# Performance work log

Measured on AMD Instinct MI355X. Metric: run time of the kernel, lower is better.

Reference implementation:

```python
import jax, jax.numpy as jnp
import numpy as np

NUM_HEADS = 8

def _ln(x):
    m = x.mean(-1, keepdims=True)
    v = ((x - m) ** 2).mean(-1, keepdims=True)
    return (x - m) / jnp.sqrt(v + 1e-5)

def _encoder_layer(x, qkv_w, out_w, w1, w2, attn_mask=None):
    # standard post-LN transformer encoder layer; returns output and
    # head-averaged attention probabilities (b, t, t)
    b, t, d = x.shape
    dh = d // NUM_HEADS
    qkv = jnp.einsum('btd,cde->cbte', x, qkv_w)          # (3, b, t, d)
    q, k, v = [a.reshape(b, t, NUM_HEADS, dh).transpose(0, 2, 1, 3) for a in qkv]
    scores = jnp.einsum('bhqd,bhkd->bhqk', q, k) / jnp.sqrt(jnp.asarray(dh, x.dtype))
    if attn_mask is not None:
        scores = scores + attn_mask                       # additive -inf/0 mask
    probs = jax.nn.softmax(scores, axis=-1)
    ctx = jnp.einsum('bhqk,bhkd->bhqd', probs, v)
    ctx = ctx.transpose(0, 2, 1, 3).reshape(b, t, d)
    x = _ln(x + ctx @ out_w)
    x = _ln(x + jax.nn.relu(x @ w1) @ w2)
    return x, probs.mean(axis=1)

def _window_ids(wbool):
    # faithful vectorization of generate_local_window_mask_v2's sequential scan:
    # run-length segmentation of the thresholded weights, where a run of
    # length 1 is absorbed into the following run (weights[frame_start] is
    # overwritten). Returns per-frame window id (T,) int32.
    T = wbool.shape[0]
    def step(carry, t):
        cur, start, wid = carry
        wt = wbool[t]
        same = wt == cur
        merge = (~same) & (start + 1 == t)   # length-1 run absorbed
        close = (~same) & (~merge)           # close window, start new one
        cur = jnp.where(same, cur, wt)
        start = jnp.where(close, t, start)
        wid = wid + close.astype(jnp.int32)
        return (cur, start, wid), wid
    _, ids = jax.lax.scan(step, (wbool[0], jnp.int32(0), jnp.int32(0)), jnp.arange(1, T))
    return jnp.concatenate([jnp.zeros((1,), jnp.int32), ids])

def reference(x, v_qkv_w, v_out_w, v_w1, v_w2, l_qkv_w, l_out_w, l_w1, l_w2):
    b, t, d = x.shape
    # 1) vanilla transformer pass
    out_v, aw_v = _encoder_layer(x, v_qkv_w, v_out_w, v_w1, v_w2)
    # attention received per key token, min-max normalized (normalize_tensor)
    w = aw_v.sum(axis=1)                                   # (b, t)
    wmin = w.min(axis=-1, keepdims=True)
    wmax = w.max(axis=-1, keepdims=True)
    w = (w - wmin) / (wmax - wmin + 1e-8)
    # 2) dynamic window mask generation (threshold = 0.5)
    ids = jax.vmap(_window_ids)(w >= 0.5)                  # (b, t)
    same = ids[:, :, None] == ids[:, None, :]
    attn_mask = jnp.where(same, 0.0, -jnp.inf).astype(x.dtype)   # (b, t, t)
    # window_mapping[b, k, j] = 1 if frame j belongs to window k
    # (kept at full t rows; torch truncates to max_window_count, which is
    #  data-dependent; extra rows here are all-zero)
    window_mapping = (jnp.arange(t, dtype=jnp.int32)[None, :, None] == ids[:, None, :]).astype(x.dtype)
    # 3) dynamic-local-window transformer pass with block-diagonal mask
    out_l, aw_l = _encoder_layer(out_v, l_qkv_w, l_out_w, l_w1, l_w2,
                                 attn_mask=attn_mask[:, None])  # broadcast over heads
    aw_l = jnp.where(jnp.isneginf(aw_l), jnp.zeros_like(aw_l), aw_l)
    wl = jax.nn.softmax(aw_l.sum(axis=1), axis=-1)         # (b, t)
    # 4) window-weighted pooling
    word_tokens = jnp.einsum('bwt,btd->bwd', window_mapping, out_l * wl[:, :, None])
    return jnp.concatenate([word_tokens, x], axis=1), window_mapping

def setup_inputs() -> dict:
    B, T, D, FF = 8, 1024, 512, 2048
    key = jax.random.key(0)
    ks = jax.random.split(key, 9)
    s = 0.02
    return {
        'x': jax.random.normal(ks[0], (B, T, D), jnp.float32),
        'v_qkv_w': jax.random.normal(ks[1], (3, D, D), jnp.float32) * s,
        'v_out_w': jax.random.normal(ks[2], (D, D), jnp.float32) * s,
        'v_w1': jax.random.normal(ks[3], (D, FF), jnp.float32) * s,
        'v_w2': jax.random.normal(ks[4], (FF, D), jnp.float32) * s,
        'l_qkv_w': jax.random.normal(ks[5], (3, D, D), jnp.float32) * s,
        'l_out_w': jax.random.normal(ks[6], (D, D), jnp.float32) * s,
        'l_w1': jax.random.normal(ks[7], (D, FF), jnp.float32) * s,
        'l_w2': jax.random.normal(ks[8], (FF, D), jnp.float32) * s,
    }
```

## Files before the change

kernel.cpp:

```cpp
#include <hip/hip_runtime.h>
#include <math.h>

#define Bz 8
#define Tz 1024
#define Dz 512
#define FFz 2048
#define Hz 8
#define DHz 64
#define Mz (Bz * Tz)

typedef __attribute__((ext_vector_type(8))) short short8;
typedef __attribute__((ext_vector_type(4))) float f32x4;

__device__ inline unsigned short f2bf(float f) {
  unsigned u = __builtin_bit_cast(unsigned, f);
  return (unsigned short)((u + 0x7FFFu + ((u >> 16) & 1u)) >> 16);
}
__device__ inline float bf2f(unsigned short h) {
  unsigned u = (unsigned)h << 16;
  return __builtin_bit_cast(float, u);
}

__device__ inline void gll16(const unsigned short* g, unsigned short* l) {
  __builtin_amdgcn_global_load_lds(
      (const __attribute__((address_space(1))) void*)g,
      (__attribute__((address_space(3))) void*)l, 16, 0, 0);
}

__device__ inline void attn_decode(int g, int& b, int& h, int& qt) {
  const int xcd = g & 7;
  const int j = g >> 3;
  qt = j & 15;
  const int bh = ((j >> 4) << 3) | xcd;
  b = bh >> 3;
  h = bh & 7;
}

__device__ inline int swz(int row, int slotByte) {
  return row * 128 + (slotByte ^ ((row & 7) << 4));
}

struct WDesc { const float* src; unsigned short* dst; unsigned short* dstlo;
               int K; int N; int blk0; };
struct PrepArgs { WDesc d[12]; int nwc; };

__global__ __launch_bounds__(256) void prep_kernel(PrepArgs P,
    const float* __restrict__ x, unsigned short* __restrict__ xbf,
    unsigned short* __restrict__ xlo, float* __restrict__ csz)
{
  const int bid = blockIdx.x;
  const int tid = threadIdx.x;
  if (bid < P.nwc) {
    int i = 0;
    while (i < 11 && bid >= P.d[i + 1].blk0) ++i;
    const WDesc w = P.d[i];
    const int lb = bid - w.blk0;
    const int nbn = w.N / 32;
    const int bn = (lb % nbn) * 32, bk = (lb / nbn) * 32;
    __shared__ float t[32][33];
    const int tx = tid & 31, ty = tid >> 5;
#pragma unroll
    for (int r = 0; r < 32; r += 8)
      t[ty + r][tx] = w.src[(size_t)(bk + ty + r) * w.N + bn + tx];
    __syncthreads();
#pragma unroll
    for (int r = 0; r < 32; r += 8) {
      float v = t[tx][ty + r];
      unsigned short hv = f2bf(v);
      w.dst[(size_t)(bn + ty + r) * w.K + bk + tx] = hv;
      if (w.dstlo)
        w.dstlo[(size_t)(bn + ty + r) * w.K + bk + tx] = f2bf(v - bf2f(hv));
    }
  } else if (bid < P.nwc + 64) {
    int idx = (bid - P.nwc) * 256 + tid;
    csz[idx] = 0.f;
  } else {
    int i = (bid - P.nwc - 64) * 256 + tid;
    float4 v = *reinterpret_cast<const float4*>(&x[(size_t)i * 4]);
    ushort4 o, ol;
    o.x = f2bf(v.x); o.y = f2bf(v.y); o.z = f2bf(v.z); o.w = f2bf(v.w);
    ol.x = f2bf(v.x - bf2f(o.x)); ol.y = f2bf(v.y - bf2f(o.y));
    ol.z = f2bf(v.z - bf2f(o.z)); ol.w = f2bf(v.w - bf2f(o.w));
    *reinterpret_cast<ushort4*>(&xbf[(size_t)i * 4]) = o;
    *reinterpret_cast<ushort4*>(&xlo[(size_t)i * 4]) = ol;
  }
}

__global__ __launch_bounds__(256) void mfma_gemm_kernel(
    const unsigned short* __restrict__ A, const unsigned short* __restrict__ BT,
    void* __restrict__ p1, void* __restrict__ p2, void* __restrict__ p3,
    int K, int N, int mode)
{
  __shared__ unsigned short As[128 * 64];
  __shared__ unsigned short Bs[128 * 64];
  const int tid = threadIdx.x;
  const int lane = tid & 63, wave = tid >> 6;
  const int mr = lane & 15, quad = lane >> 4;
  const int wr = wave >> 1, wc = wave & 1;
  const int m0 = blockIdx.y * 128;
  const int n0 = blockIdx.x * 128;

  f32x4 acc[4][4];
  const f32x4 zero = {0.f, 0.f, 0.f, 0.f};
#pragma unroll
  for (int i = 0; i < 4; ++i)
#pragma unroll
    for (int j = 0; j < 4; ++j) acc[i][j] = zero;

  const int r8 = lane >> 3;
  const int s8 = (lane & 7) ^ r8;
  const unsigned short* Agb = A + (size_t)(m0 + wave * 8 + r8) * K + s8 * 8;
  const unsigned short* Bgb = BT + (size_t)(n0 + wave * 8 + r8) * K + s8 * 8;
  unsigned short* Adb = As + wave * 512;
  unsigned short* Bdb = Bs + wave * 512;
  char* AsB = (char*)As;
  char* BsB = (char*)Bs;
  const int xr = (mr & 7) << 4;

  for (int k0 = 0; k0 < K; k0 += 64) {
#pragma unroll
    for (int p = 0; p < 4; ++p) {
      gll16(Agb + (size_t)(p * 32) * K + k0, Adb + p * 2048);
      gll16(Bgb + (size_t)(p * 32) * K + k0, Bdb + p * 2048);
    }
    __syncthreads();
    short8 af[2][4], bf[2][4];
#pragma unroll
    for (int hh = 0; hh < 2; ++hh) {
#pragma unroll
      for (int i = 0; i < 4; ++i)
        af[hh][i] = *reinterpret_cast<const short8*>(
            AsB + (wr * 64 + i * 16 + mr) * 128 + ((((hh << 2) + quad) << 4) ^ xr));
#pragma unroll
      for (int j = 0; j < 4; ++j)
        bf[hh][j] = *reinterpret_cast<const short8*>(
            BsB + (wc * 64 + j * 16 + mr) * 128 + ((((hh << 2) + quad) << 4) ^ xr));
    }
#pragma unroll
    for (int hh = 0; hh < 2; ++hh)
#pragma unroll
      for (int i = 0; i < 4; ++i)
#pragma unroll
        for (int j = 0; j < 4; ++j)
          acc[i][j] = __builtin_amdgcn_mfma_f32_16x16x32_bf16(af[hh][i], bf[hh][j], acc[i][j], 0, 0, 0);
    __syncthreads();
  }

  const int m0w = m0 + wr * 64;
  const int n0w = n0 + wc * 64;
  int emode = mode;
  unsigned short* Cbf = (unsigned short*)p1;
  unsigned short* Vt  = (unsigned short*)p1;
  int ncol = N, coff = 0;
  if (mode == 5) {
    if (n0w < 512)       { emode = 1; Cbf = (unsigned short*)p1; ncol = 512; coff = 0; }
    else if (n0w < 1024) { emode = 1; Cbf = (unsigned short*)p2; ncol = 512; coff = 512; }
    else                 { emode = 4; Vt = (unsigned short*)p3; coff = 1024; }
  }
  if (emode == 4) {
#pragma unroll
    for (int i = 0; i < 4; ++i)
#pragma unroll
      for (int j = 0; j < 4; ++j) {
        const int col = n0w - coff + j * 16 + mr;
        const int row0 = m0w + i * 16 + quad * 4;
        const int bb = row0 >> 10, t0 = row0 & 1023;
        ushort4 pk;
        pk.x = f2bf(acc[i][j][0]); pk.y = f2bf(acc[i][j][1]);
        pk.z = f2bf(acc[i][j][2]); pk.w = f2bf(acc[i][j][3]);
        *reinterpret_cast<ushort4*>(
            &Vt[((size_t)((bb * Hz + (col >> 6)) * DHz + (col & 63))) * Tz + t0]) = pk;
      }
  } else if (emode == 0) {
    float* Cf = (float*)p1;
#pragma unroll
    for (int i = 0; i < 4; ++i)
#pragma unroll
      for (int j = 0; j < 4; ++j) {
        const int col = n0w + j * 16 + mr;
#pragma unroll
        for (int rr = 0; rr < 4; ++rr)
          Cf[(size_t)(m0w + i * 16 + quad * 4 + rr) * N + col] = acc[i][j][rr];
      }
  } else {
    const bool relu = (emode == 2);
#pragma unroll
    for (int i = 0; i < 4; ++i)
#pragma unroll
      for (int j = 0; j < 4; ++j) {
        const int col = n0w - coff + j * 16 + mr;
#pragma unroll
        for (int rr = 0; rr < 4; ++rr) {
          float v = acc[i][j][rr];
          if (relu) v = fmaxf(v, 0.f);
          Cbf[(size_t)(m0w + i * 16 + quad * 4 + rr) * ncol + col] = f2bf(v);
        }
      }
  }
}

__global__ __launch_bounds__(256) void gemm_qk_mfma_kernel(
    const unsigned short* __restrict__ Xh, const unsigned short* __restrict__ Xl,
    const unsigned short* __restrict__ WQh, const unsigned short* __restrict__ WQl,
    const unsigned short* __restrict__ WKh, const unsigned short* __restrict__ WKl,
    unsigned short* __restrict__ Qhi, unsigned short* __restrict__ Qlo,
    unsigned short* __restrict__ Khi, unsigned short* __restrict__ Klo)
{
  __shared__ unsigned short Ash[128 * 64];
  __shared__ unsigned short Asl[128 * 64];
  __shared__ unsigned short Bsh[128 * 64];
  __shared__ unsigned short Bsl[128 * 64];
  const int tid = threadIdx.x;
  const int lane = tid & 63, wave = tid >> 6;
  const int mr = lane & 15, quad = lane >> 4;
  const int wr = wave >> 1, wc = wave & 1;
  const int sel = blockIdx.y >> 6;
  const int m0 = (blockIdx.y & 63) * 128;
  const int n0 = blockIdx.x * 128;
  const unsigned short* Bh = sel ? WKh : WQh;
  const unsigned short* Bl = sel ? WKl : WQl;
  unsigned short* Chi = sel ? Khi : Qhi;
  unsigned short* Clo = sel ? Klo : Qlo;

  f32x4 acc[4][4];
  const f32x4 zero = {0.f, 0.f, 0.f, 0.f};
#pragma unroll
  for (int i = 0; i < 4; ++i)
#pragma unroll
    for (int j = 0; j < 4; ++j) acc[i][j] = zero;

  const int r8 = lane >> 3;
  const int s8 = (lane & 7) ^ r8;
  const unsigned short* gAh = Xh + (size_t)(m0 + wave * 8 + r8) * Dz + s8 * 8;
  const unsigned short* gAl = Xl + (size_t)(m0 + wave * 8 + r8) * Dz + s8 * 8;
  const unsigned short* gBh = Bh + (size_t)(n0 + wave * 8 + r8) * Dz + s8 * 8;
  const unsigned short* gBl = Bl + (size_t)(n0 + wave * 8 + r8) * Dz + s8 * 8;
  unsigned short* dAh = Ash + wave * 512;
  unsigned short* dAl = Asl + wave * 512;
  unsigned short* dBh = Bsh + wave * 512;
  unsigned short* dBl = Bsl + wave * 512;
  char* AhB = (char*)Ash; char* AlB = (char*)Asl;
  char* BhB = (char*)Bsh; char* BlB = (char*)Bsl;
  const int xr = (mr & 7) << 4;

  for (int k0 = 0; k0 < Dz; k0 += 64) {
#pragma unroll
    for (int p = 0; p < 4; ++p) {
      gll16(gAh + (size_t)(p * 32) * Dz + k0, dAh + p * 2048);
      gll16(gAl + (size_t)(p * 32) * Dz + k0, dAl + p * 2048);
      gll16(gBh + (size_t)(p * 32) * Dz + k0, dBh + p * 2048);
      gll16(gBl + (size_t)(p * 32) * Dz + k0, dBl + p * 2048);
    }
    __syncthreads();
    short8 ah[2][4], al[2][4], bh[2][4], bl[2][4];
#pragma unroll
    for (int hh = 0; hh < 2; ++hh) {
#pragma unroll
      for (int i = 0; i < 4; ++i) {
        const int ab = (wr * 64 + i * 16 + mr) * 128 + ((((hh << 2) + quad) << 4) ^ xr);
        ah[hh][i] = *reinterpret_cast<const short8*>(AhB + ab);
        al[hh][i] = *reinterpret_cast<const short8*>(AlB + ab);
      }
#pragma unroll
      for (int j = 0; j < 4; ++j) {
        const int bb = (wc * 64 + j * 16 + mr) * 128 + ((((hh << 2) + quad) << 4) ^ xr);
        bh[hh][j] = *reinterpret_cast<const short8*>(BhB + bb);
        bl[hh][j] = *reinterpret_cast<const short8*>(BlB + bb);
      }
    }
#pragma unroll
    for (int hh = 0; hh < 2; ++hh)
#pragma unroll
      for (int i = 0; i < 4; ++i)
#pragma unroll
        for (int j = 0; j < 4; ++j) {
          acc[i][j] = __builtin_amdgcn_mfma_f32_16x16x32_bf16(al[hh][i], bh[hh][j], acc[i][j], 0, 0, 0);
          acc[i][j] = __builtin_amdgcn_mfma_f32_16x16x32_bf16(ah[hh][i], bl[hh][j], acc[i][j], 0, 0, 0);
          acc[i][j] = __builtin_amdgcn_mfma_f32_16x16x32_bf16(ah[hh][i], bh[hh][j], acc[i][j], 0, 0, 0);
        }
    __syncthreads();
  }

  const int m0w = m0 + wr * 64;
  const int n0w = n0 + wc * 64;
#pragma unroll
  for (int i = 0; i < 4; ++i)
#pragma unroll
    for (int j = 0; j < 4; ++j) {
      const int col = n0w + j * 16 + mr;
#pragma unroll
      for (int rr = 0; rr < 4; ++rr) {
        const size_t row = (size_t)(m0w + i * 16 + quad * 4 + rr);
        float v = acc[i][j][rr];
        unsigned short hv = f2bf(v);
        Chi[row * Dz + col] = hv;
        Clo[row * Dz + col] = f2bf(v - bf2f(hv));
      }
    }
}

__global__ __launch_bounds__(256) void attn_fused_kernel(
    const unsigned short* __restrict__ Qh, const unsigned short* __restrict__ Ql,
    const unsigned short* __restrict__ Kh, const unsigned short* __restrict__ Kl,
    const unsigned short* __restrict__ Vt,
    unsigned short* __restrict__ ctx, float* __restrict__ part)
{
  __shared__ unsigned short Ksh[64 * 64];
  __shared__ unsigned short Ksl[64 * 64];
  __shared__ unsigned short Vsh[64 * 64];
  __shared__ unsigned short Pld[64][76];
  __shared__ float CSPt[4][64];
  const int tid = threadIdx.x;
  const int lane = tid & 63, wave = tid >> 6;
  const int c = lane & 15, quad = lane >> 4;
  int b, h, qt;
  attn_decode(blockIdx.x, b, h, qt);
  const size_t bT = (size_t)b * Tz;
  const int qrow = qt * 64 + wave * 16;
  const int hoff = h * DHz;
  const int lidx = b * 128 + h * 16 + qt;

  const size_t qbase = (bT + qrow + c) * Dz + hoff + quad * 8;
  short8 q0h = *reinterpret_cast<const short8*>(Qh + qbase);
  short8 q1h = *reinterpret_cast<const short8*>(Qh + qbase + 32);
  short8 q0l = *reinterpret_cast<const short8*>(Ql + qbase);
  short8 q1l = *reinterpret_cast<const short8*>(Ql + qbase + 32);

  const int r8 = lane >> 3;
  const int s8 = (lane & 7) ^ r8;
  const unsigned short* khg = Kh + (bT + wave * 8 + r8) * Dz + hoff + s8 * 8;
  const unsigned short* klg = Kl + (bT + wave * 8 + r8) * Dz + hoff + s8 * 8;
  const unsigned short* vtg = Vt + ((size_t)((b * Hz + h) * DHz) + wave * 8 + r8) * Tz + s8 * 8;
  unsigned short* KshW = Ksh + wave * 512;
  unsigned short* KslW = Ksl + wave * 512;
  unsigned short* VshW = Vsh + wave * 512;
  char* KshB = (char*)Ksh;
  char* KslB = (char*)Ksl;
  char* VshB = (char*)Vsh;

  const f32x4 zf = {0.f, 0.f, 0.f, 0.f};

  float z[4] = {0.f, 0.f, 0.f, 0.f};
  for (int t = 0; t < 16; ++t) {
    const int k0 = t * 64;
    gll16(khg + (size_t)k0 * Dz, KshW);
    gll16(khg + (size_t)(k0 + 32) * Dz, KshW + 2048);
    __syncthreads();
#pragma unroll
    for (int sub = 0; sub < 4; ++sub) {
      const int row = sub * 16 + c;
      short8 kh0 = *reinterpret_cast<const short8*>(KshB + swz(row, quad * 16));
      short8 kh1 = *reinterpret_cast<const short8*>(KshB + swz(row, 64 + quad * 16));
      f32x4 aA = zf, aB = zf;
      aA = __builtin_amdgcn_mfma_f32_16x16x32_bf16(q0h, kh0, aA, 0, 0, 0);
      aB = __builtin_amdgcn_mfma_f32_16x16x32_bf16(q1h, kh1, aB, 0, 0, 0);
#pragma unroll
      for (int rr = 0; rr < 4; ++rr) z[rr] += __expf((aA[rr] + aB[rr]) * 0.125f);
    }
    __syncthreads();
  }
#pragma unroll
  for (int w = 1; w < 16; w <<= 1) {
#pragma unroll
    for (int rr = 0; rr < 4; ++rr) z[rr] += __shfl_xor(z[rr], w);
  }
  float invz[4];
#pragma unroll
  for (int rr = 0; rr < 4; ++rr) invz[rr] = 1.f / z[rr];

  f32x4 ot[4] = {zf, zf, zf, zf};
  for (int t = 0; t < 16; ++t) {
    const int k0 = t * 64;
    gll16(khg + (size_t)k0 * Dz, KshW);
    gll16(khg + (size_t)(k0 + 32) * Dz, KshW + 2048);
    gll16(klg + (size_t)k0 * Dz, KslW);
    gll16(klg + (size_t)(k0 + 32) * Dz, KslW + 2048);
    gll16(vtg + k0, VshW);
    gll16(vtg + (size_t)32 * Tz + k0, VshW + 2048);
    __syncthreads();

#pragma unroll
    for (int sub = 0; sub < 4; ++sub) {
      const int row = sub * 16 + c;
      short8 kh0 = *reinterpret_cast<const short8*>(KshB + swz(row, quad * 16));
      short8 kh1 = *reinterpret_cast<const short8*>(KshB + swz(row, 64 + quad * 16));
      short8 kl0 = *reinterpret_cast<const short8*>(KslB + swz(row, quad * 16));
      short8 kl1 = *reinterpret_cast<const short8*>(KslB + swz(row, 64 + quad * 16));
      f32x4 aA = zf, aB = zf;
      aA = __builtin_amdgcn_mfma_f32_16x16x32_bf16(q0h, kh0, aA, 0, 0, 0);
      aB = __builtin_amdgcn_mfma_f32_16x16x32_bf16(q1h, kh1, aB, 0, 0, 0);
      aA = __builtin_amdgcn_mfma_f32_16x16x32_bf16(q0h, kl0, aA, 0, 0, 0);
      aB = __builtin_amdgcn_mfma_f32_16x16x32_bf16(q1h, kl1, aB, 0, 0, 0);
      aA = __builtin_amdgcn_mfma_f32_16x16x32_bf16(q0l, kh0, aA, 0, 0, 0);
      aB = __builtin_amdgcn_mfma_f32_16x16x32_bf16(q1l, kh1, aB, 0, 0, 0);
      float p[4];
#pragma unroll
      for (int rr = 0; rr < 4; ++rr)
        p[rr] = __expf((aA[rr] + aB[rr]) * 0.125f) * invz[rr];
      float cs = p[0] + p[1] + p[2] + p[3];
      cs += __shfl_xor(cs, 16);
      cs += __shfl_xor(cs, 32);
      if (quad == 0) CSPt[wave][sub * 16 + c] = cs;
#pragma unroll
      for (int rr = 0; rr < 4; ++rr)
        Pld[(wave << 4) + quad * 4 + rr][sub * 16 + c] = f2bf(p[rr]);
    }

    union { short8 v; ushort4 hh[2]; } pb0, pb1;
    pb0.hh[0] = *reinterpret_cast<const ushort4*>(&Pld[(wave << 4) + c][quad * 8]);
    pb0.hh[1] = *reinterpret_cast<const ushort4*>(&Pld[(wave << 4) + c][quad * 8 + 4]);
    pb1.hh[0] = *reinterpret_cast<const ushort4*>(&Pld[(wave << 4) + c][32 + quad * 8]);
    pb1.hh[1] = *reinterpret_cast<const ushort4*>(&Pld[(wave << 4) + c][32 + quad * 8 + 4]);
#pragma unroll
    for (int ds = 0; ds < 4; ++ds) {
      const int row = ds * 16 + c;
      short8 v0 = *reinterpret_cast<const short8*>(VshB + swz(row, quad * 16));
      short8 v1 = *reinterpret_cast<const short8*>(VshB + swz(row, 64 + quad * 16));
      ot[ds] = __builtin_amdgcn_mfma_f32_16x16x32_bf16(v0, pb0.v, ot[ds], 0, 0, 0);
      ot[ds] = __builtin_amdgcn_mfma_f32_16x16x32_bf16(v1, pb1.v, ot[ds], 0, 0, 0);
    }
    __syncthreads();

    if (tid < 64) {
      float v = ((CSPt[0][tid] + CSPt[1][tid]) + CSPt[2][tid]) + CSPt[3][tid];
      part[(size_t)lidx * 1024 + k0 + tid] = v * (1.f / Hz);
    }
  }

  const size_t cb = (bT + qrow + c) * Dz + hoff;
#pragma unroll
  for (int ds = 0; ds < 4; ++ds) {
    ushort4 pk;
    pk.x = f2bf(ot[ds][0]); pk.y = f2bf(ot[ds][1]);
    pk.z = f2bf(ot[ds][2]); pk.w = f2bf(ot[ds][3]);
    *reinterpret_cast<ushort4*>(&ctx[cb + ds * 16 + quad * 4]) = pk;
  }
}

__global__ __launch_bounds__(256) void colsum_reduce_kernel(
    const float* __restrict__ part, float* __restrict__ colsum)
{
  const int i = blockIdx.x * 256 + threadIdx.x;
  const int b = i >> 10, k = i & 1023;
  const float* p = part + (size_t)(b * 128) * 1024 + k;
  float s = 0.f;
  for (int j = 0; j < 128; ++j) s += p[(size_t)j * 1024];
  colsum[i] = s;
}

__global__ __launch_bounds__(256) void attn_mfma2_kernel(
    const unsigned short* __restrict__ Qh, const unsigned short* __restrict__ Kh,
    const unsigned short* __restrict__ Vt, const int* __restrict__ ids,
    const int* __restrict__ wst,
    unsigned short* __restrict__ ctx, float* __restrict__ colsum)
{
  __shared__ unsigned short Ksh[64 * 64];
  __shared__ unsigned short Vsh[64 * 64];
  __shared__ unsigned short Pld[64][76];
  __shared__ float csb[1024];

  const int tid = threadIdx.x;
  const int lane = tid & 63, wave = tid >> 6;
  const int c = lane & 15, quad = lane >> 4;
  int b, h, qt;
  attn_decode(blockIdx.x, b, h, qt);
  const size_t bT = (size_t)b * Tz;
  const int qrow = qt * 64 + wave * 16;
  const int hoff = h * DHz;

  for (int i = tid; i < 1024; i += 256) csb[i] = 0.f;

  const int id_lo = ids[bT + qt * 64];
  const int id_hi = ids[bT + qt * 64 + 63];
  const int klo = wst[b * (Tz + 1) + id_lo];
  const int khi = wst[b * (Tz + 1) + id_hi + 1];
  const int t0 = klo >> 6, t1 = (khi - 1) >> 6;

  const size_t qbase = (bT + qrow + c) * Dz + hoff + quad * 8;
  short8 q0 = *reinterpret_cast<const short8*>(Qh + qbase);
  short8 q1 = *reinterpret_cast<const short8*>(Qh + qbase + 32);

  int qid[4];
#pragma unroll
  for (int rr = 0; rr < 4; ++rr) qid[rr] = ids[bT + qrow + quad * 4 + rr];

  const int r8 = lane >> 3;
  const int s8 = (lane & 7) ^ r8;
  const unsigned short* khg = Kh + (bT + wave * 8 + r8) * Dz + hoff + s8 * 8;
  const unsigned short* vtg = Vt + ((size_t)((b * Hz + h) * DHz) + wave * 8 + r8) * Tz + s8 * 8;
  unsigned short* KshW = Ksh + wave * 512;
  unsigned short* VshW = Vsh + wave * 512;
  char* KshB = (char*)Ksh;
  char* VshB = (char*)Vsh;
  __syncthreads();

  const f32x4 zf = {0.f, 0.f, 0.f, 0.f};

  float z[4] = {0.f, 0.f, 0.f, 0.f};
  for (int t = t0; t <= t1; ++t) {
    const int k0 = t * 64;
    gll16(khg + (size_t)k0 * Dz, KshW);
    gll16(khg + (size_t)(k0 + 32) * Dz, KshW + 2048);
    __syncthreads();
#pragma unroll
    for (int sub = 0; sub < 4; ++sub) {
      const int row = sub * 16 + c;
      short8 kh0 = *reinterpret_cast<const short8*>(KshB + swz(row, quad * 16));
      short8 kh1 = *reinterpret_cast<const short8*>(KshB + swz(row, 64 + quad * 16));
      f32x4 acc = zf;
      acc = __builtin_amdgcn_mfma_f32_16x16x32_bf16(q0, kh0, acc, 0, 0, 0);
      acc = __builtin_amdgcn_mfma_f32_16x16x32_bf16(q1, kh1, acc, 0, 0, 0);
      int kidv = ids[bT + k0 + sub * 16 + c];
#pragma unroll
      for (int rr = 0; rr < 4; ++rr) {
        float e = __expf(acc[rr] * 0.125f);
        if (qid[rr] != kidv) e = 0.f;
        z[rr] += e;
      }
    }
    __syncthreads();
  }
#pragma unroll
  for (int w = 1; w < 16; w <<= 1) {
#pragma unroll
    for (int rr = 0; rr < 4; ++rr) z[rr] += __shfl_xor(z[rr], w);
  }
  float invz[4];
#pragma unroll
  for (int rr = 0; rr < 4; ++rr) invz[rr] = 1.f / z[rr];

  f32x4 ot[4] = {zf, zf, zf, zf};
  for (int t = t0; t <= t1; ++t) {
    const int k0 = t * 64;
    gll16(khg + (size_t)k0 * Dz, KshW);
    gll16(khg + (size_t)(k0 + 32) * Dz, KshW + 2048);
    gll16(vtg + k0, VshW);
    gll16(vtg + (size_t)32 * Tz + k0, VshW + 2048);
    __syncthreads();
#pragma unroll
    for (int sub = 0; sub < 4; ++sub) {
      const int row = sub * 16 + c;
      short8 kh0 = *reinterpret_cast<const short8*>(KshB + swz(row, quad * 16));
      short8 kh1 = *reinterpret_cast<const short8*>(KshB + swz(row, 64 + quad * 16));
      f32x4 acc = zf;
      acc = __builtin_amdgcn_mfma_f32_16x16x32_bf16(q0, kh0, acc, 0, 0, 0);
      acc = __builtin_amdgcn_mfma_f32_16x16x32_bf16(q1, kh1, acc, 0, 0, 0);
      int kidv = ids[bT + k0 + sub * 16 + c];
      float p[4];
#pragma unroll
      for (int rr = 0; rr < 4; ++rr) {
        float e = __expf(acc[rr] * 0.125f);
        if (qid[rr] != kidv) e = 0.f;
        p[rr] = e * invz[rr];
      }
      float cs = p[0] + p[1] + p[2] + p[3];
      cs += __shfl_xor(cs, 16);
      cs += __shfl_xor(cs, 32);
      if (quad == 0) atomicAdd(&csb[k0 + sub * 16 + c], cs);
#pragma unroll
      for (int rr = 0; rr < 4; ++rr)
        Pld[(wave << 4) + quad * 4 + rr][sub * 16 + c] = f2bf(p[rr]);
    }
    union { short8 v; ushort4 hh[2]; } pb0, pb1;
    pb0.hh[0] = *reinterpret_cast<const ushort4*>(&Pld[(wave << 4) + c][quad * 8]);
    pb0.hh[1] = *reinterpret_cast<const ushort4*>(&Pld[(wave << 4) + c][quad * 8 + 4]);
    pb1.hh[0] = *reinterpret_cast<const ushort4*>(&Pld[(wave << 4) + c][32 + quad * 8]);
    pb1.hh[1] = *reinterpret_cast<const ushort4*>(&Pld[(wave << 4) + c][32 + quad * 8 + 4]);
#pragma unroll
    for (int ds = 0; ds < 4; ++ds) {
      const int row = ds * 16 + c;
      short8 v0 = *reinterpret_cast<const short8*>(VshB + swz(row, quad * 16));
      short8 v1 = *reinterpret_cast<const short8*>(VshB + swz(row, 64 + quad * 16));
      ot[ds] = __builtin_amdgcn_mfma_f32_16x16x32_bf16(v0, pb0.v, ot[ds], 0, 0, 0);
      ot[ds] = __builtin_amdgcn_mfma_f32_16x16x32_bf16(v1, pb1.v, ot[ds], 0, 0, 0);
    }
    __syncthreads();
  }

  const size_t cb = (bT + qrow + c) * Dz + hoff;
#pragma unroll
  for (int ds = 0; ds < 4; ++ds) {
    ushort4 pk;
    pk.x = f2bf(ot[ds][0]); pk.y = f2bf(ot[ds][1]);
    pk.z = f2bf(ot[ds][2]); pk.w = f2bf(ot[ds][3]);
    *reinterpret_cast<ushort4*>(&ctx[cb + ds * 16 + quad * 4]) = pk;
  }
  __syncthreads();
  for (int i = tid; i < 1024; i += 256)
    atomicAdd(&colsum[bT + i], csb[i] * (1.f / Hz));
}

__global__ __launch_bounds__(256) void ln_kernel(const float* __restrict__ residf,
    const unsigned short* __restrict__ residbf, const float* __restrict__ delta,
    float* __restrict__ outf, unsigned short* __restrict__ outbf)
{
  const size_t base = (size_t)blockIdx.x * Dz;
  const int tid = threadIdx.x;
  float r0, r1;
  if (residf) {
    r0 = residf[base + tid]; r1 = residf[base + tid + 256];
  } else {
    r0 = bf2f(residbf[base + tid]); r1 = bf2f(residbf[base + tid + 256]);
  }
  float x0 = r0 + delta[base + tid];
  float x1 = r1 + delta[base + tid + 256];
  __shared__ float red[4];
  float s = x0 + x1;
#pragma unroll
  for (int off = 32; off; off >>= 1) s += __shfl_down(s, off);
  if ((tid & 63) == 0) red[tid >> 6] = s;
  __syncthreads();
  const float mean = (red[0] + red[1] + red[2] + red[3]) * (1.f / Dz);
  __syncthreads();
  float d0 = x0 - mean, d1 = x1 - mean;
  float v = d0 * d0 + d1 * d1;
#pragma unroll
  for (int off = 32; off; off >>= 1) v += __shfl_down(v, off);
  if ((tid & 63) == 0) red[tid >> 6] = v;
  __syncthreads();
  const float var = (red[0] + red[1] + red[2] + red[3]) * (1.f / Dz);
  const float rstd = rsqrtf(var + 1e-5f);
  float y0 = d0 * rstd, y1 = d1 * rstd;
  if (outf) {
    outf[base + tid] = y0;
    outf[base + tid + 256] = y1;
  }
  outbf[base + tid] = f2bf(y0);
  outbf[base + tid + 256] = f2bf(y1);
}

__global__ __launch_bounds__(256) void window_ids_kernel(const float* __restrict__ cs,
    int* __restrict__ ids, int* __restrict__ wst, int* __restrict__ nwin)
{
  const int b = blockIdx.x, tid = threadIdx.x;
  __shared__ float vals[Tz];
  __shared__ int swst[Tz + 1];
  __shared__ unsigned long long words[16];
  __shared__ float rmin[4], rmax[4];
  __shared__ int snw;
  float mn = INFINITY, mx = -INFINITY;
  for (int t = tid; t < Tz; t += 256) {
    float v = cs[b * Tz + t];
    vals[t] = v;
    mn = fminf(mn, v); mx = fmaxf(mx, v);
  }
#pragma unroll
  for (int off = 32; off; off >>= 1) {
    mn = fminf(mn, __shfl_down(mn, off));
    mx = fmaxf(mx, __shfl_down(mx, off));
  }
  if ((tid & 63) == 0) { rmin[tid >> 6] = mn; rmax[tid >> 6] = mx; }
  __syncthreads();
  mn = fminf(fminf(rmin[0], rmin[1]), fminf(rmin[2], rmin[3]));
  mx = fmaxf(fmaxf(rmax[0], rmax[1]), fmaxf(rmax[2], rmax[3]));
  const float inv = 1.f / (mx - mn + 1e-8f);
  const int lane = tid & 63, wave = tid >> 6;
#pragma unroll
  for (int pass = 0; pass < 4; ++pass) {
    const int t = pass * 256 + wave * 64 + lane;
    const bool bit = ((vals[t] - mn) * inv) >= 0.5f;
    unsigned long long m = __ballot(bit);
    if (lane == 0) words[pass * 4 + wave] = m;
  }
  __syncthreads();
  if (tid == 0) {
    int start = 0, wid = 0;
    swst[0] = 0;
    unsigned long long carry = 0;
    for (int i = 0; i < 16; ++i) {
      const unsigned long long wi = words[i];
      unsigned long long tr = wi ^ ((wi << 1) | carry);
      carry = wi >> 63;
      if (i == 0) tr &= ~1ULL;
      while (tr) {
        const int t = i * 64 + __builtin_ctzll(tr);
        tr &= tr - 1;
        if (start + 1 != t) { start = t; ++wid; swst[wid] = t; }
      }
    }
    nwin[b] = wid + 1;
    swst[wid + 1] = Tz;
    snw = wid + 1;
  }
  __syncthreads();
  const int nw = snw;
  for (int j = tid; j <= nw; j += 256) wst[b * (Tz + 1) + j] = swst[j];
  for (int t = tid; t < Tz; t += 256) {
    int lo = 0, hi = nw;
    while (hi - lo > 1) {
      const int mid = (lo + hi) >> 1;
      if (swst[mid] <= t) lo = mid; else hi = mid;
    }
    ids[b * Tz + t] = lo;
  }
}

__global__ __launch_bounds__(256) void wl_softmax_kernel(const float* __restrict__ cs,
                                                         float* __restrict__ wl)
{
  const int b = blockIdx.x, tid = threadIdx.x;
  __shared__ float vals[Tz];
  __shared__ float red[4];
  float mx = -INFINITY;
  for (int t = tid; t < Tz; t += 256) {
    float v = cs[b * Tz + t];
    vals[t] = v;
    mx = fmaxf(mx, v);
  }
#pragma unroll
  for (int off = 32; off; off >>= 1) mx = fmaxf(mx, __shfl_down(mx, off));
  if ((tid & 63) == 0) red[tid >> 6] = mx;
  __syncthreads();
  mx = fmaxf(fmaxf(red[0], red[1]), fmaxf(red[2], red[3]));
  __syncthreads();
  float se = 0.f;
  for (int t = tid; t < Tz; t += 256) {
    float e = expf(vals[t] - mx);
    vals[t] = e;
    se += e;
  }
#pragma unroll
  for (int off = 32; off; off >>= 1) se += __shfl_down(se, off);
  if ((tid & 63) == 0) red[tid >> 6] = se;
  __syncthreads();
  const float inv = 1.f / (red[0] + red[1] + red[2] + red[3]);
  for (int t = tid; t < Tz; t += 256) wl[b * Tz + t] = vals[t] * inv;
}

__global__ __launch_bounds__(256) void outputs_kernel(
    const unsigned short* __restrict__ outl, const float* __restrict__ wl,
    const int* __restrict__ wst, const int* __restrict__ nwin,
    const int* __restrict__ ids, const float* __restrict__ x,
    float* __restrict__ out, float* __restrict__ out2)
{
  const int bid = blockIdx.x;
  const int tid = threadIdx.x;
  if (bid < 8192) {
    const int w = bid & (Tz - 1);
    const int b = bid >> 10;
    float a0 = 0.f, a1 = 0.f;
    if (w < nwin[b]) {
      const int s = wst[b * (Tz + 1) + w], e = wst[b * (Tz + 1) + w + 1];
      for (int t = s; t < e; ++t) {
        const float sc = wl[b * Tz + t];
        const unsigned short* p = &outl[((size_t)(b * Tz + t)) * Dz];
        a0 += bf2f(p[tid]) * sc;
        a1 += bf2f(p[tid + 256]) * sc;
      }
    }
    float* o = &out[((size_t)(b * 2 * Tz + w)) * Dz];
    o[tid] = a0;
    o[tid + 256] = a1;
  } else if (bid < 16384) {
    const int lb = bid - 8192;
    const int w = lb & (Tz - 1);
    const int b = lb >> 10;
    const int j = tid * 4;
    int4 id4 = *reinterpret_cast<const int4*>(&ids[b * Tz + j]);
    float4 v;
    v.x = (id4.x == w) ? 1.f : 0.f;
    v.y = (id4.y == w) ? 1.f : 0.f;
    v.z = (id4.z == w) ? 1.f : 0.f;
    v.w = (id4.w == w) ? 1.f : 0.f;
    *reinterpret_cast<float4*>(&out2[((size_t)(b * Tz + w)) * Tz + j]) = v;
  } else {
    size_t i = (size_t)(bid - 16384) * 256 + tid;
    size_t idx = i * 4;
    size_t rowi = idx >> 9;
    size_t d = idx & 511;
    size_t b = rowi >> 10, t = rowi & 1023;
    float4 v = *reinterpret_cast<const float4*>(&x[idx]);
    *reinterpret_cast<float4*>(&out[(((b * 2 * Tz) + Tz + t) << 9) + d]) = v;
  }
}

extern "C" void kernel_launch(void* const* d_in, const int* in_sizes, int n_in,
                              void* d_out, int out_size, void* d_ws, size_t ws_size,
                              hipStream_t stream)
{
  (void)in_sizes; (void)n_in; (void)out_size; (void)ws_size;
  const float* x     = (const float*)d_in[0];
  const float* vqkv  = (const float*)d_in[1];
  const float* voutw = (const float*)d_in[2];
  const float* vw1   = (const float*)d_in[3];
  const float* vw2   = (const float*)d_in[4];
  const float* lqkv  = (const float*)d_in[5];
  const float* loutw = (const float*)d_in[6];
  const float* lw1   = (const float*)d_in[7];
  const float* lw2   = (const float*)d_in[8];
  float* out = (float*)d_out;
  float* ws  = (float*)d_ws;

  unsigned short* QLbf = (unsigned short*)(ws + 0);
  unsigned short* KLbf = (unsigned short*)(ws + 2097152);
  float* PROJ = ws + 0;
  float* Y1   = ws + 4194304;
  unsigned short* QHbf = (unsigned short*)(ws + 8388608);
  unsigned short* KHbf = (unsigned short*)(ws + 10485760);
  unsigned short* VT   = (unsigned short*)(ws + 12582912);
  unsigned short* SLOT1 = (unsigned short*)(ws + 14680064);
  unsigned short* SLOT2 = (unsigned short*)(ws + 16777216);
  unsigned short* HIDbf = (unsigned short*)(ws + 18874368);
  unsigned short* XBF   = (unsigned short*)(ws + 18874368);
  float* PART = ws + 18874368;
  unsigned short* XLO = (unsigned short*)(ws + 20971520);
  unsigned short* WVQV = (unsigned short*)(ws + 27262976);
  unsigned short* WVO  = (unsigned short*)(ws + 27394048);
  unsigned short* WV1  = (unsigned short*)(ws + 27525120);
  unsigned short* WV2  = (unsigned short*)(ws + 28049408);
  unsigned short* WLQ0 = (unsigned short*)(ws + 28573696);
  unsigned short* WLQ1 = (unsigned short*)(ws + 28704768);
  unsigned short* WLQ2 = (unsigned short*)(ws + 28835840);
  unsigned short* WLO  = (unsigned short*)(ws + 28966912);
  unsigned short* WL1  = (unsigned short*)(ws + 29097984);
  unsigned short* WL2  = (unsigned short*)(ws + 29622272);
  float* CS1   = ws + 30146560;
  float* CS2   = ws + 30154752;
  float* WLs   = ws + 30162944;
  int*   IDS   = (int*)(ws + 30171136);
  int*   WST   = (int*)(ws + 30179328);
  int*   NWIN  = (int*)(ws + 30187776);
  unsigned short* WQH = (unsigned short*)(ws + 30261504);
  unsigned short* WQL = (unsigned short*)(ws + 30392576);
  unsigned short* WKH = (unsigned short*)(ws + 30523648);
  unsigned short* WKL = (unsigned short*)(ws + 30654720);

  dim3 blk(256);

  PrepArgs P;
  auto setw = [&](int i, const float* s, unsigned short* d, unsigned short* dl,
                  int K, int N, int b0) {
    P.d[i].src = s; P.d[i].dst = d; P.d[i].dstlo = dl;
    P.d[i].K = K; P.d[i].N = N; P.d[i].blk0 = b0;
  };
  int b0 = 0;
  setw(0, vqkv + 2 * Dz * Dz, WVQV, nullptr, Dz, Dz, b0); b0 += 256;
  setw(1, voutw, WVO, nullptr, Dz, Dz, b0); b0 += 256;
  setw(2, vw1, WV1, nullptr, Dz, FFz, b0); b0 += 1024;
  setw(3, vw2, WV2, nullptr, FFz, Dz, b0); b0 += 1024;
  setw(4, lqkv + 0 * Dz * Dz, WLQ0, nullptr, Dz, Dz, b0); b0 += 256;
  setw(5, lqkv + 1 * Dz * Dz, WLQ1, nullptr, Dz, Dz, b0); b0 += 256;
  setw(6, lqkv + 2 * Dz * Dz, WLQ2, nullptr, Dz, Dz, b0); b0 += 256;
  setw(7, loutw, WLO, nullptr, Dz, Dz, b0); b0 += 256;
  setw(8, lw1, WL1, nullptr, Dz, FFz, b0); b0 += 1024;
  setw(9, lw2, WL2, nullptr, FFz, Dz, b0); b0 += 1024;
  setw(10, vqkv + 0 * Dz * Dz, WQH, WQL, Dz, Dz, b0); b0 += 256;
  setw(11, vqkv + 1 * Dz * Dz, WKH, WKL, Dz, Dz, b0); b0 += 256;
  P.nwc = b0;
  prep_kernel<<<dim3(P.nwc + 64 + 4096), blk, 0, stream>>>(P, x, XBF, XLO, CS1);

  auto mgemm = [&](const unsigned short* A, const unsigned short* BT, void* p1,
                   void* p2, void* p3, int K, int N, int mode) {
    mfma_gemm_kernel<<<dim3(N / 128, Mz / 128), dim3(256), 0, stream>>>(
        A, BT, p1, p2, p3, K, N, mode);
  };

  gemm_qk_mfma_kernel<<<dim3(4, 128), dim3(256), 0, stream>>>(
      XBF, XLO, WQH, WQL, WKH, WKL, QHbf, QLbf, KHbf, KLbf);
  mgemm(XBF, WVQV, VT, nullptr, nullptr, Dz, Dz, 4);
  attn_fused_kernel<<<dim3(Bz * Hz * 16), blk, 0, stream>>>(
      QHbf, QLbf, KHbf, KLbf, VT, SLOT1, PART);
  colsum_reduce_kernel<<<dim3(32), blk, 0, stream>>>(PART, CS1);
  window_ids_kernel<<<dim3(Bz), blk, 0, stream>>>(CS1, IDS, WST, NWIN);
  mgemm(SLOT1, WVO, PROJ, nullptr, nullptr, Dz, Dz, 0);
  ln_kernel<<<dim3(Mz), blk, 0, stream>>>(x, nullptr, PROJ, Y1, SLOT2);
  mgemm(SLOT2, WV1, HIDbf, nullptr, nullptr, Dz, FFz, 2);
  mgemm(HIDbf, WV2, PROJ, nullptr, nullptr, FFz, Dz, 0);
  ln_kernel<<<dim3(Mz), blk, 0, stream>>>(Y1, nullptr, PROJ, nullptr, SLOT2);

  mgemm(SLOT2, WLQ0, QHbf, KHbf, VT, Dz, 3 * Dz, 5);
  attn_mfma2_kernel<<<dim3(Bz * Hz * 16), blk, 0, stream>>>(
      QHbf, KHbf, VT, IDS, WST, SLOT1, CS2);
  mgemm(SLOT1, WLO, PROJ, nullptr, nullptr, Dz, Dz, 0);
  ln_kernel<<<dim3(Mz), blk, 0, stream>>>(nullptr, SLOT2, PROJ, Y1, SLOT2);
  mgemm(SLOT2, WL1, HIDbf, nullptr, nullptr, Dz, FFz, 2);
  mgemm(HIDbf, WL2, PROJ, nullptr, nullptr, FFz, Dz, 0);
  ln_kernel<<<dim3(Mz), blk, 0, stream>>>(Y1, nullptr, PROJ, nullptr, SLOT2);

  wl_softmax_kernel<<<dim3(Bz), blk, 0, stream>>>(CS2, WLs);
  outputs_kernel<<<dim3(20480), blk, 0, stream>>>(SLOT2, WLs, WST, NWIN, IDS, x,
                                                  out, out + (size_t)Bz * 2 * Tz * Dz);
}
```

Measured before the change: 540.1 us.

## Add MFMA wave priority hints, halve z-pass barriers, fuse colsum into window ids

Wraps the MFMA sections of the GEMM and attention kernels in s_setprio(1)/s_setprio(0), so waves issuing matrix ops get scheduling priority over waves issuing loads. The first attention pass now loads 128 keys per iteration into both LDS buffers, which halves its barrier count. The separate column-sum reduction kernel is merged into window_ids_kernel, removing one launch. The trade-off is that the merged reduction runs on only 8 blocks, which serialises 128 strided reads per column per thread.

```diff
diff --git a/kernel.cpp b/kernel.cpp
--- a/kernel.cpp
+++ b/kernel.cpp
@@ -136,6 +136,7 @@
         bf[hh][j] = *reinterpret_cast<const short8*>(
             BsB + (wc * 64 + j * 16 + mr) * 128 + ((((hh << 2) + quad) << 4) ^ xr));
     }
+    __builtin_amdgcn_s_setprio(1);
 #pragma unroll
     for (int hh = 0; hh < 2; ++hh)
 #pragma unroll
@@ -143,6 +144,7 @@
 #pragma unroll
         for (int j = 0; j < 4; ++j)
           acc[i][j] = __builtin_amdgcn_mfma_f32_16x16x32_bf16(af[hh][i], bf[hh][j], acc[i][j], 0, 0, 0);
+    __builtin_amdgcn_s_setprio(0);
     __syncthreads();
   }
 
@@ -268,6 +270,7 @@
         bl[hh][j] = *reinterpret_cast<const short8*>(BlB + bb);
       }
     }
+    __builtin_amdgcn_s_setprio(1);
 #pragma unroll
     for (int hh = 0; hh < 2; ++hh)
 #pragma unroll
@@ -278,6 +281,7 @@
           acc[i][j] = __builtin_amdgcn_mfma_f32_16x16x32_bf16(ah[hh][i], bl[hh][j], acc[i][j], 0, 0, 0);
           acc[i][j] = __builtin_amdgcn_mfma_f32_16x16x32_bf16(ah[hh][i], bh[hh][j], acc[i][j], 0, 0, 0);
         }
+    __builtin_amdgcn_s_setprio(0);
     __syncthreads();
   }
 
@@ -341,22 +345,30 @@
   const f32x4 zf = {0.f, 0.f, 0.f, 0.f};
 
   float z[4] = {0.f, 0.f, 0.f, 0.f};
-  for (int t = 0; t < 16; ++t) {
-    const int k0 = t * 64;
+  for (int tt = 0; tt < 8; ++tt) {
+    const int k0 = tt * 128;
     gll16(khg + (size_t)k0 * Dz, KshW);
     gll16(khg + (size_t)(k0 + 32) * Dz, KshW + 2048);
-    __syncthreads();
-#pragma unroll
-    for (int sub = 0; sub < 4; ++sub) {
-      const int row = sub * 16 + c;
-      short8 kh0 = *reinterpret_cast<const short8*>(KshB + swz(row, quad * 16));
-      short8 kh1 = *reinterpret_cast<const short8*>(KshB + swz(row, 64 + quad * 16));
-      f32x4 aA = zf, aB = zf;
-      aA = __builtin_amdgcn_mfma_f32_16x16x32_bf16(q0h, kh0, aA, 0, 0, 0);
-      aB = __builtin_amdgcn_mfma_f32_16x16x32_bf16(q1h, kh1, aB, 0, 0, 0);
-#pragma unroll
-      for (int rr = 0; rr < 4; ++rr) z[rr] += __expf((aA[rr] + aB[rr]) * 0.125f);
-    }
+    gll16(khg + (size_t)(k0 + 64) * Dz, KslW);
+    gll16(khg + (size_t)(k0 + 96) * Dz, KslW + 2048);
+    __syncthreads();
+    __builtin_amdgcn_s_setprio(1);
+#pragma unroll
+    for (int half = 0; half < 2; ++half) {
+      char* Kb = half ? KslB : KshB;
+#pragma unroll
+      for (int sub = 0; sub < 4; ++sub) {
+        const int row = sub * 16 + c;
+        short8 kh0 = *reinterpret_cast<const short8*>(Kb + swz(row, quad * 16));
+        short8 kh1 = *reinterpret_cast<const short8*>(Kb + swz(row, 64 + quad * 16));
+        f32x4 aA = zf, aB = zf;
+        aA = __builtin_amdgcn_mfma_f32_16x16x32_bf16(q0h, kh0, aA, 0, 0, 0);
+        aB = __builtin_amdgcn_mfma_f32_16x16x32_bf16(q1h, kh1, aB, 0, 0, 0);
+#pragma unroll
+        for (int rr = 0; rr < 4; ++rr) z[rr] += __expf((aA[rr] + aB[rr]) * 0.125f);
+      }
+    }
+    __builtin_amdgcn_s_setprio(0);
     __syncthreads();
   }
 #pragma unroll
@@ -387,12 +399,14 @@
       short8 kl0 = *reinterpret_cast<const short8*>(KslB + swz(row, quad * 16));
       short8 kl1 = *reinterpret_cast<const short8*>(KslB + swz(row, 64 + quad * 16));
       f32x4 aA = zf, aB = zf;
+      __builtin_amdgcn_s_setprio(1);
       aA = __builtin_amdgcn_mfma_f32_16x16x32_bf16(q0h, kh0, aA, 0, 0, 0);
       aB = __builtin_amdgcn_mfma_f32_16x16x32_bf16(q1h, kh1, aB, 0, 0, 0);
       aA = __builtin_amdgcn_mfma_f32_16x16x32_bf16(q0h, kl0, aA, 0, 0, 0);
       aB = __builtin_amdgcn_mfma_f32_16x16x32_bf16(q1h, kl1, aB, 0, 0, 0);
       aA = __builtin_amdgcn_mfma_f32_16x16x32_bf16(q0l, kh0, aA, 0, 0, 0);
       aB = __builtin_amdgcn_mfma_f32_16x16x32_bf16(q1l, kh1, aB, 0, 0, 0);
+      __builtin_amdgcn_s_setprio(0);
       float p[4];
 #pragma unroll
       for (int rr = 0; rr < 4; ++rr)
@@ -411,6 +425,7 @@
     pb0.hh[1] = *reinterpret_cast<const ushort4*>(&Pld[(wave << 4) + c][quad * 8 + 4]);
     pb1.hh[0] = *reinterpret_cast<const ushort4*>(&Pld[(wave << 4) + c][32 + quad * 8]);
     pb1.hh[1] = *reinterpret_cast<const ushort4*>(&Pld[(wave << 4) + c][32 + quad * 8 + 4]);
+    __builtin_amdgcn_s_setprio(1);
 #pragma unroll
     for (int ds = 0; ds < 4; ++ds) {
       const int row = ds * 16 + c;
@@ -419,6 +434,7 @@
       ot[ds] = __builtin_amdgcn_mfma_f32_16x16x32_bf16(v0, pb0.v, ot[ds], 0, 0, 0);
       ot[ds] = __builtin_amdgcn_mfma_f32_16x16x32_bf16(v1, pb1.v, ot[ds], 0, 0, 0);
     }
+    __builtin_amdgcn_s_setprio(0);
     __syncthreads();
 
     if (tid < 64) {
@@ -435,17 +451,6 @@
     pk.z = f2bf(ot[ds][2]); pk.w = f2bf(ot[ds][3]);
     *reinterpret_cast<ushort4*>(&ctx[cb + ds * 16 + quad * 4]) = pk;
   }
-}
-
-__global__ __launch_bounds__(256) void colsum_reduce_kernel(
-    const float* __restrict__ part, float* __restrict__ colsum)
-{
-  const int i = blockIdx.x * 256 + threadIdx.x;
-  const int b = i >> 10, k = i & 1023;
-  const float* p = part + (size_t)(b * 128) * 1024 + k;
-  float s = 0.f;
-  for (int j = 0; j < 128; ++j) s += p[(size_t)j * 1024];
-  colsum[i] = s;
 }
 
 __global__ __launch_bounds__(256) void attn_mfma2_kernel(
@@ -502,6 +507,7 @@
     gll16(khg + (size_t)k0 * Dz, KshW);
     gll16(khg + (size_t)(k0 + 32) * Dz, KshW + 2048);
     __syncthreads();
+    __builtin_amdgcn_s_setprio(1);
 #pragma unroll
     for (int sub = 0; sub < 4; ++sub) {
       const int row = sub * 16 + c;
@@ -518,6 +524,7 @@
         z[rr] += e;
       }
     }
+    __builtin_amdgcn_s_setprio(0);
     __syncthreads();
   }
 #pragma unroll
@@ -543,8 +550,10 @@
       short8 kh0 = *reinterpret_cast<const short8*>(KshB + swz(row, quad * 16));
       short8 kh1 = *reinterpret_cast<const short8*>(KshB + swz(row, 64 + quad * 16));
       f32x4 acc = zf;
+      __builtin_amdgcn_s_setprio(1);
       acc = __builtin_amdgcn_mfma_f32_16x16x32_bf16(q0, kh0, acc, 0, 0, 0);
       acc = __builtin_amdgcn_mfma_f32_16x16x32_bf16(q1, kh1, acc, 0, 0, 0);
+      __builtin_amdgcn_s_setprio(0);
       int kidv = ids[bT + k0 + sub * 16 + c];
       float p[4];
 #pragma unroll
@@ -566,6 +575,7 @@
     pb0.hh[1] = *reinterpret_cast<const ushort4*>(&Pld[(wave << 4) + c][quad * 8 + 4]);
     pb1.hh[0] = *reinterpret_cast<const ushort4*>(&Pld[(wave << 4) + c][32 + quad * 8]);
     pb1.hh[1] = *reinterpret_cast<const ushort4*>(&Pld[(wave << 4) + c][32 + quad * 8 + 4]);
+    __builtin_amdgcn_s_setprio(1);
 #pragma unroll
     for (int ds = 0; ds < 4; ++ds) {
       const int row = ds * 16 + c;
@@ -574,6 +584,7 @@
       ot[ds] = __builtin_amdgcn_mfma_f32_16x16x32_bf16(v0, pb0.v, ot[ds], 0, 0, 0);
       ot[ds] = __builtin_amdgcn_mfma_f32_16x16x32_bf16(v1, pb1.v, ot[ds], 0, 0, 0);
     }
+    __builtin_amdgcn_s_setprio(0);
     __syncthreads();
   }
 
@@ -629,7 +640,7 @@
   outbf[base + tid + 256] = f2bf(y1);
 }
 
-__global__ __launch_bounds__(256) void window_ids_kernel(const float* __restrict__ cs,
+__global__ __launch_bounds__(256) void window_ids_kernel(const float* __restrict__ part,
     int* __restrict__ ids, int* __restrict__ wst, int* __restrict__ nwin)
 {
   const int b = blockIdx.x, tid = threadIdx.x;
@@ -638,10 +649,16 @@
   __shared__ unsigned long long words[16];
   __shared__ float rmin[4], rmax[4];
   __shared__ int snw;
+  for (int k = tid; k < Tz; k += 256) {
+    const float* p = part + (size_t)(b * 128) * 1024 + k;
+    float s = 0.f;
+    for (int j = 0; j < 128; ++j) s += p[(size_t)j * 1024];
+    vals[k] = s;
+  }
+  __syncthreads();
   float mn = INFINITY, mx = -INFINITY;
   for (int t = tid; t < Tz; t += 256) {
-    float v = cs[b * Tz + t];
-    vals[t] = v;
+    float v = vals[t];
     mn = fminf(mn, v); mx = fmaxf(mx, v);
   }
 #pragma unroll
@@ -860,8 +877,7 @@
   mgemm(XBF, WVQV, VT, nullptr, nullptr, Dz, Dz, 4);
   attn_fused_kernel<<<dim3(Bz * Hz * 16), blk, 0, stream>>>(
       QHbf, QLbf, KHbf, KLbf, VT, SLOT1, PART);
-  colsum_reduce_kernel<<<dim3(32), blk, 0, stream>>>(PART, CS1);
-  window_ids_kernel<<<dim3(Bz), blk, 0, stream>>>(CS1, IDS, WST, NWIN);
+  window_ids_kernel<<<dim3(Bz), blk, 0, stream>>>(PART, IDS, WST, NWIN);
   mgemm(SLOT1, WVO, PROJ, nullptr, nullptr, Dz, Dz, 0);
   ln_kernel<<<dim3(Mz), blk, 0, stream>>>(x, nullptr, PROJ, Y1, SLOT2);
   mgemm(SLOT2, WV1, HIDbf, nullptr, nullptr, Dz, FFz, 2);
```

After: 569.2 us. 1.05x slower.
